# Optimization experiments

Hardware: AMD Instinct MI355X
Metric: run time of the kernel (lower is better)

Reference implementation:

```python
import jax, jax.numpy as jnp
import numpy as np

PRIOR_HOURS = 48.0
INIT_TIME = 0.0
K = 13  # nr_ref_time_points (time_space)
L = 200  # time steps (axis_2)
D = 64   # features (axis_3)
B = 64

REF_TIME = jnp.asarray(np.linspace(INIT_TIME, PRIOR_HOURS, K).reshape(K, 1, 1), dtype=jnp.float32)


def setup_inputs() -> dict:
    key = jax.random.key(0)
    ks = jax.random.split(key, 9)
    X = jax.random.normal(ks[0], (B, L, D), dtype=jnp.float32)
    T = jax.random.uniform(ks[1], (B, L, D), dtype=jnp.float32) * PRIOR_HOURS
    M = (jax.random.uniform(ks[2], (B, L, D)) > 0.5).astype(jnp.float32)
    DT = jax.random.uniform(ks[3], (B, L, D), dtype=jnp.float32)
    # trainable weights (keras random_normal initializer, stddev=0.05)
    alpha = jax.random.normal(ks[4], (K, 1, 1), dtype=jnp.float32) * 0.05
    w_v = jax.random.normal(ks[5], (K, L, D), dtype=jnp.float32) * 0.05
    w_t = jax.random.normal(ks[6], (K, L, D, 4), dtype=jnp.float32) * 0.05
    b_v = jax.random.normal(ks[7], (K, 1, D), dtype=jnp.float32) * 0.05
    b_t = jax.random.normal(ks[8], (K, L, D, 1), dtype=jnp.float32) * 0.05
    return {"X": X, "T": T, "M": M, "DT": DT, "alpha": alpha,
            "w_v": w_v, "w_t": w_t, "b_v": b_v, "b_t": b_t}


def reference(X, T, M, DT, alpha, w_v, w_t, b_v, b_t):
    # broadcast inputs over the K reference time points: [B,1,L,D] -> [B,K,L,D]
    dist = jnp.abs(T[:, None, :, :] - REF_TIME)                 # [B,K,L,D]
    kernel = jnp.exp(-jax.nn.relu(alpha) * dist)                # [B,K,L,D]
    intensity = jax.nn.relu(X[:, None, :, :] * kernel)          # [B,K,L,D]
    shp = intensity.shape
    x = jnp.broadcast_to(X[:, None, :, :], shp)
    dt = jnp.broadcast_to(DT[:, None, :, :], shp)
    m = jnp.broadcast_to(M[:, None, :, :], shp)
    feat = jnp.stack([x, dt, intensity, m], axis=-1)            # [B,K,L,D,4]
    # stage 1: weighted reduce over the 4-feature axis (b_t broadcasts over it)
    lat = jax.nn.relu(jnp.sum(w_t * feat + b_t, axis=-1))       # [B,K,L,D]
    # stage 2: weighted reduce over the time-step axis L (b_v broadcasts over it)
    out = jax.nn.relu(jnp.sum(w_v * lat + b_v, axis=2))         # [B,K,D]
    return out
```

## Files before the change

kernel.cpp:

```cpp
#include <hip/hip_runtime.h>


#define NB 64
#define NK 13
#define NL 200
#define ND 64
#define ND4 16
#define GB 8
#define LC 4
#define NC (NL / LC)

__global__ __launch_bounds__(256) void alnn_stage1(
    const float* __restrict__ X, const float* __restrict__ T,
    const float* __restrict__ M, const float* __restrict__ DT,
    const float* __restrict__ alpha, const float* __restrict__ w_v,
    const float* __restrict__ w_t, const float* __restrict__ b_t,
    float4* __restrict__ part)
{
    const int bid = blockIdx.x;
    const int xcd = bid & 7;
    const int j   = bid >> 3;
    const int c   = ((j >> 3) << 3) | xcd;
    if (c >= NC) return;
    const int bg  = j & 7;

    const int tid = threadIdx.x;
    const int dq  = tid & 15;
    const int s   = tid >> 4;
    const int bb  = s >> 1;
    const int lh  = s & 1;
    const int b   = (bg << 3) + bb;
    const int la  = c * LC + (lh << 1);
    const int d0  = dq << 2;

    const float4* X4  = (const float4*)X;
    const float4* T4  = (const float4*)T;
    const float4* M4  = (const float4*)M;
    const float4* DT4 = (const float4*)DT;
    const float4* WT4 = (const float4*)w_t;
    const float4* BT4 = (const float4*)b_t;
    const float4* WV4 = (const float4*)w_v;

    const int io0 = (b * NL + la) * ND4 + dq;
    const int io1 = io0 + ND4;
    const float4 xA = X4[io0],  xB = X4[io1];
    const float4 tA = T4[io0],  tB = T4[io1];
    const float4 mA = M4[io0],  mB = M4[io1];
    const float4 dA = DT4[io0], dB = DT4[io1];

    float4 acc[NK];
    #pragma unroll
    for (int k = 0; k < NK; ++k) acc[k] = make_float4(0.f, 0.f, 0.f, 0.f);

#define COMP(c_, wt, xv, tv, mv, dv, bt4, wv4, A) {                       \
        const float dist  = fabsf(tv.c_ - reft);                          \
        const float inten = fmaxf(xv.c_ * __expf(-a * dist), 0.f);        \
        const float sf = wt.x * xv.c_ + wt.y * dv.c_ + wt.z * inten +     \
                         wt.w * mv.c_ + 4.f * bt4.c_;                     \
        A.c_ = fmaf(wv4.c_, fmaxf(sf, 0.f), A.c_);                        \
    }

    #pragma unroll
    for (int k = 0; k < NK; ++k) {
        const float a    = fmaxf(alpha[k], 0.f);
        const float reft = 4.f * (float)k;
        const int wq = (k * NL + la) * ND4 + dq;
        const int w0 = (k * NL + la) * ND + d0;
        {
            const float4 wt0 = WT4[w0 + 0];
            const float4 wt1 = WT4[w0 + 1];
            const float4 wt2 = WT4[w0 + 2];
            const float4 wt3 = WT4[w0 + 3];
            const float4 bt4 = BT4[wq];
            const float4 wv4 = WV4[wq];
            COMP(x, wt0, xA, tA, mA, dA, bt4, wv4, acc[k])
            COMP(y, wt1, xA, tA, mA, dA, bt4, wv4, acc[k])
            COMP(z, wt2, xA, tA, mA, dA, bt4, wv4, acc[k])
            COMP(w, wt3, xA, tA, mA, dA, bt4, wv4, acc[k])
        }
        {
            const float4 wt0 = WT4[w0 + ND + 0];
            const float4 wt1 = WT4[w0 + ND + 1];
            const float4 wt2 = WT4[w0 + ND + 2];
            const float4 wt3 = WT4[w0 + ND + 3];
            const float4 bt4 = BT4[wq + ND4];
            const float4 wv4 = WV4[wq + ND4];
            COMP(x, wt0, xB, tB, mB, dB, bt4, wv4, acc[k])
            COMP(y, wt1, xB, tB, mB, dB, bt4, wv4, acc[k])
            COMP(z, wt2, xB, tB, mB, dB, bt4, wv4, acc[k])
            COMP(w, wt3, xB, tB, mB, dB, bt4, wv4, acc[k])
        }
    }
#undef COMP

    #pragma unroll
    for (int k = 0; k < NK; ++k) {
        acc[k].x += __shfl_xor(acc[k].x, 16);
        acc[k].y += __shfl_xor(acc[k].y, 16);
        acc[k].z += __shfl_xor(acc[k].z, 16);
        acc[k].w += __shfl_xor(acc[k].w, 16);
    }

    const int pb = ((c * NB + b) * NK) * ND4 + dq;
    #pragma unroll
    for (int k = 0; k < NK; ++k) {
        if ((k < 7) == (lh == 0))
            part[pb + k * ND4] = acc[k];
    }
}

__global__ __launch_bounds__(256) void alnn_stage2(
    const float4* __restrict__ part, const float* __restrict__ b_v,
    float4* __restrict__ out)
{
    const int tid = blockIdx.x * 256 + threadIdx.x;
    const int dq  = tid & 15;
    const int bk  = tid >> 4;
    const int k   = bk % NK;

    float4 s = make_float4(0.f, 0.f, 0.f, 0.f);
    #pragma unroll 5
    for (int c = 0; c < NC; ++c) {
        const float4 p = part[(c * NB * NK + bk) * ND4 + dq];
        s.x += p.x; s.y += p.y; s.z += p.z; s.w += p.w;
    }
    const float4 bv = ((const float4*)b_v)[k * ND4 + dq];
    float4 r;
    r.x = fmaxf(s.x + 200.f * bv.x, 0.f);
    r.y = fmaxf(s.y + 200.f * bv.y, 0.f);
    r.z = fmaxf(s.z + 200.f * bv.z, 0.f);
    r.w = fmaxf(s.w + 200.f * bv.w, 0.f);
    out[tid] = r;
}

extern "C" void kernel_launch(void* const* d_in, const int* in_sizes, int n_in,
                              void* d_out, int out_size, void* d_ws, size_t ws_size,
                              hipStream_t stream) {
    const float* X     = (const float*)d_in[0];
    const float* T     = (const float*)d_in[1];
    const float* M     = (const float*)d_in[2];
    const float* DT    = (const float*)d_in[3];
    const float* alpha = (const float*)d_in[4];
    const float* w_v   = (const float*)d_in[5];
    const float* w_t   = (const float*)d_in[6];
    const float* b_v   = (const float*)d_in[7];
    const float* b_t   = (const float*)d_in[8];

    float4* part = (float4*)d_ws;

    alnn_stage1<<<512, 256, 0, stream>>>(X, T, M, DT, alpha, w_v, w_t, b_t, part);
    alnn_stage2<<<(NB * NK * ND4) / 256, 256, 0, stream>>>(part, b_v, (float4*)d_out);
}
```

Before: 100.7 us.

## Split stage1 work over K halves with smaller L chunks; parallelize stage2 reduction

Stage 1 now processes 2 time steps per block and splits the 13 reference times across the two halves of each block (7 and 6 k values), instead of splitting L across thread pairs and combining them with a shuffle. This doubles the number of L chunks and so the grid grows to 832 blocks. Stage 2 splits the longer chunk reduction four ways per output and combines the partial sums with cross-lane shuffles. The intent is more parallelism and shorter dependency chains, in exchange for twice the partial-sum workspace traffic and uneven work between the k halves.

```diff
diff --git a/kernel.cpp b/kernel.cpp
--- a/kernel.cpp
+++ b/kernel.cpp
@@ -7,7 +7,7 @@
 #define ND 64
 #define ND4 16
 #define GB 8
-#define LC 4
+#define LC 2
 #define NC (NL / LC)
 
 __global__ __launch_bounds__(256) void alnn_stage1(
@@ -18,20 +18,20 @@
     float4* __restrict__ part)
 {
     const int bid = blockIdx.x;
-    const int xcd = bid & 7;
-    const int j   = bid >> 3;
-    const int c   = ((j >> 3) << 3) | xcd;
+    const int clo = bid & 7;
+    const int g   = bid >> 3;
+    const int bg  = g & 7;
+    const int chi = g >> 3;
+    const int c   = chi * 8 + clo;
     if (c >= NC) return;
-    const int bg  = j & 7;
 
     const int tid = threadIdx.x;
     const int dq  = tid & 15;
-    const int s   = tid >> 4;
-    const int bb  = s >> 1;
-    const int lh  = s & 1;
-    const int b   = (bg << 3) + bb;
-    const int la  = c * LC + (lh << 1);
-    const int d0  = dq << 2;
+    const int b8  = (tid >> 4) & 7;
+    const int ks  = tid >> 7;
+    const int k0  = ks * 7;
+    const int b   = (bg << 3) + b8;
+    const int la  = c * LC;
 
     const float4* X4  = (const float4*)X;
     const float4* T4  = (const float4*)T;
@@ -41,96 +41,96 @@
     const float4* BT4 = (const float4*)b_t;
     const float4* WV4 = (const float4*)w_v;
 
-    const int io0 = (b * NL + la) * ND4 + dq;
-    const int io1 = io0 + ND4;
-    const float4 xA = X4[io0],  xB = X4[io1];
-    const float4 tA = T4[io0],  tB = T4[io1];
-    const float4 mA = M4[io0],  mB = M4[io1];
-    const float4 dA = DT4[io0], dB = DT4[io1];
+    float av[7], rv[7];
+    #pragma unroll
+    for (int i = 0; i < 7; ++i) {
+        const int k = k0 + i;
+        av[i] = (k < NK) ? fmaxf(alpha[k], 0.f) : 0.f;
+        rv[i] = 4.f * (float)k;
+    }
 
-    float4 acc[NK];
+    float4 acc[7];
     #pragma unroll
-    for (int k = 0; k < NK; ++k) acc[k] = make_float4(0.f, 0.f, 0.f, 0.f);
+    for (int i = 0; i < 7; ++i) acc[i] = make_float4(0.f, 0.f, 0.f, 0.f);
 
-#define COMP(c_, wt, xv, tv, mv, dv, bt4, wv4, A) {                       \
-        const float dist  = fabsf(tv.c_ - reft);                          \
-        const float inten = fmaxf(xv.c_ * __expf(-a * dist), 0.f);        \
-        const float sf = wt.x * xv.c_ + wt.y * dv.c_ + wt.z * inten +     \
-                         wt.w * mv.c_ + 4.f * bt4.c_;                     \
+#define COMP(c_, wt, A) {                                                 \
+        const float dist  = fabsf(t4.c_ - reft);                          \
+        const float inten = fmaxf(x4.c_ * __expf(-a * dist), 0.f);        \
+        const float sf = wt.x * x4.c_ + wt.y * dt4.c_ + wt.z * inten +    \
+                         wt.w * m4.c_ + 4.f * bt4.c_;                     \
         A.c_ = fmaf(wv4.c_, fmaxf(sf, 0.f), A.c_);                        \
     }
 
     #pragma unroll
-    for (int k = 0; k < NK; ++k) {
-        const float a    = fmaxf(alpha[k], 0.f);
-        const float reft = 4.f * (float)k;
-        const int wq = (k * NL + la) * ND4 + dq;
-        const int w0 = (k * NL + la) * ND + d0;
-        {
-            const float4 wt0 = WT4[w0 + 0];
-            const float4 wt1 = WT4[w0 + 1];
-            const float4 wt2 = WT4[w0 + 2];
-            const float4 wt3 = WT4[w0 + 3];
-            const float4 bt4 = BT4[wq];
-            const float4 wv4 = WV4[wq];
-            COMP(x, wt0, xA, tA, mA, dA, bt4, wv4, acc[k])
-            COMP(y, wt1, xA, tA, mA, dA, bt4, wv4, acc[k])
-            COMP(z, wt2, xA, tA, mA, dA, bt4, wv4, acc[k])
-            COMP(w, wt3, xA, tA, mA, dA, bt4, wv4, acc[k])
-        }
-        {
-            const float4 wt0 = WT4[w0 + ND + 0];
-            const float4 wt1 = WT4[w0 + ND + 1];
-            const float4 wt2 = WT4[w0 + ND + 2];
-            const float4 wt3 = WT4[w0 + ND + 3];
-            const float4 bt4 = BT4[wq + ND4];
-            const float4 wv4 = WV4[wq + ND4];
-            COMP(x, wt0, xB, tB, mB, dB, bt4, wv4, acc[k])
-            COMP(y, wt1, xB, tB, mB, dB, bt4, wv4, acc[k])
-            COMP(z, wt2, xB, tB, mB, dB, bt4, wv4, acc[k])
-            COMP(w, wt3, xB, tB, mB, dB, bt4, wv4, acc[k])
+    for (int li = 0; li < LC; ++li) {
+        const int l  = la + li;
+        const int io = (b * NL + l) * ND4 + dq;
+        const float4 x4  = X4[io];
+        const float4 t4  = T4[io];
+        const float4 m4  = M4[io];
+        const float4 dt4 = DT4[io];
+        #pragma unroll
+        for (int i = 0; i < 7; ++i) {
+            const int k = k0 + i;
+            if (k < NK) {
+                const int w0 = (k * NL + l) * ND + (dq << 2);
+                const float4 wt0 = WT4[w0 + 0];
+                const float4 wt1 = WT4[w0 + 1];
+                const float4 wt2 = WT4[w0 + 2];
+                const float4 wt3 = WT4[w0 + 3];
+                const int   wq  = (k * NL + l) * ND4 + dq;
+                const float4 bt4 = BT4[wq];
+                const float4 wv4 = WV4[wq];
+                const float a    = av[i];
+                const float reft = rv[i];
+                COMP(x, wt0, acc[i])
+                COMP(y, wt1, acc[i])
+                COMP(z, wt2, acc[i])
+                COMP(w, wt3, acc[i])
+            }
         }
     }
 #undef COMP
 
+    const int pb = ((c * NB + b) * NK + k0) * ND4 + dq;
     #pragma unroll
-    for (int k = 0; k < NK; ++k) {
-        acc[k].x += __shfl_xor(acc[k].x, 16);
-        acc[k].y += __shfl_xor(acc[k].y, 16);
-        acc[k].z += __shfl_xor(acc[k].z, 16);
-        acc[k].w += __shfl_xor(acc[k].w, 16);
-    }
-
-    const int pb = ((c * NB + b) * NK) * ND4 + dq;
-    #pragma unroll
-    for (int k = 0; k < NK; ++k) {
-        if ((k < 7) == (lh == 0))
-            part[pb + k * ND4] = acc[k];
-    }
+    for (int i = 0; i < 7; ++i)
+        if (k0 + i < NK) part[pb + i * ND4] = acc[i];
 }
 
 __global__ __launch_bounds__(256) void alnn_stage2(
     const float4* __restrict__ part, const float* __restrict__ b_v,
     float4* __restrict__ out)
 {
-    const int tid = blockIdx.x * 256 + threadIdx.x;
-    const int dq  = tid & 15;
-    const int bk  = tid >> 4;
-    const int k   = bk % NK;
+    const int g  = blockIdx.x * 256 + threadIdx.x;
+    const int dq = g & 15;
+    const int r  = g >> 4;
+    const int q  = r & 3;
+    const int bk = r >> 2;
+    if (bk >= NB * NK) return;
 
     float4 s = make_float4(0.f, 0.f, 0.f, 0.f);
     #pragma unroll 5
-    for (int c = 0; c < NC; ++c) {
+    for (int i = 0; i < NC / 4; ++i) {
+        const int c = q * (NC / 4) + i;
         const float4 p = part[(c * NB * NK + bk) * ND4 + dq];
         s.x += p.x; s.y += p.y; s.z += p.z; s.w += p.w;
     }
-    const float4 bv = ((const float4*)b_v)[k * ND4 + dq];
-    float4 r;
-    r.x = fmaxf(s.x + 200.f * bv.x, 0.f);
-    r.y = fmaxf(s.y + 200.f * bv.y, 0.f);
-    r.z = fmaxf(s.z + 200.f * bv.z, 0.f);
-    r.w = fmaxf(s.w + 200.f * bv.w, 0.f);
-    out[tid] = r;
+    s.x += __shfl_xor(s.x, 16); s.y += __shfl_xor(s.y, 16);
+    s.z += __shfl_xor(s.z, 16); s.w += __shfl_xor(s.w, 16);
+    s.x += __shfl_xor(s.x, 32); s.y += __shfl_xor(s.y, 32);
+    s.z += __shfl_xor(s.z, 32); s.w += __shfl_xor(s.w, 32);
+
+    if (q == 0) {
+        const int k = bk % NK;
+        const float4 bv = ((const float4*)b_v)[k * ND4 + dq];
+        float4 o;
+        o.x = fmaxf(s.x + 200.f * bv.x, 0.f);
+        o.y = fmaxf(s.y + 200.f * bv.y, 0.f);
+        o.z = fmaxf(s.z + 200.f * bv.z, 0.f);
+        o.w = fmaxf(s.w + 200.f * bv.w, 0.f);
+        out[bk * ND4 + dq] = o;
+    }
 }
 
 extern "C" void kernel_launch(void* const* d_in, const int* in_sizes, int n_in,
@@ -148,6 +148,6 @@
 
     float4* part = (float4*)d_ws;
 
-    alnn_stage1<<<512, 256, 0, stream>>>(X, T, M, DT, alpha, w_v, w_t, b_t, part);
-    alnn_stage2<<<(NB * NK * ND4) / 256, 256, 0, stream>>>(part, b_v, (float4*)d_out);
+    alnn_stage1<<<832, 256, 0, stream>>>(X, T, M, DT, alpha, w_v, w_t, b_t, part);
+    alnn_stage2<<<(NB * NK * 64) / 256, 256, 0, stream>>>(part, b_v, (float4*)d_out);
 }
```

After: 101.4 us. About the same (+0.7%).
